# Kernel optimization log

Measured on AMD Instinct MI355X. Metric: run time of the kernel, lower is better.

The kernel has to match this reference:

```python
import jax, jax.numpy as jnp
import numpy as np

T = 8192  # context/question length (input_shape[2])
D = 128   # feature dim (input_shape[3])


def setup_inputs() -> dict:
    key = jax.random.key(0)
    k1, k2 = jax.random.split(key)
    x = jax.random.normal(k1, (2, 1, T, D), dtype=jnp.float32)
    kernel = jax.random.normal(k2, (3 * D,), dtype=jnp.float32)
    return {"x": x, "kernel": kernel}


def reference(x, kernel):
    context = x[0, 0]   # (T, D)
    question = x[1, 0]  # (T, D)
    w_c, w_q, w_m = kernel[:D], kernel[D:2 * D], kernel[2 * D:]

    # Additive similarity: S[i,j] = c_i.w_c + q_j.w_q + (c_i*q_j).w_m
    # Avoids materializing the (T, T, 3D) tiled/concatenated tensor.
    S = (context @ w_c)[:, None] + (question @ w_q)[None, :] \
        + (context * w_m) @ question.T  # (T, T)

    A = jax.nn.softmax(S, axis=-1)  # row-wise softmax, as tf.nn.softmax on 2D

    # C2Q attention: U_A[i] = sum_j A[i,j] * q_j
    U_A = A @ question  # (T, D)

    # Q2C attention: b = row-max of A, h = sum_i b_i * c_i, tiled over rows
    b = jnp.max(A, axis=1)          # (T,)
    h = b @ context                 # (D,)
    H_A = jnp.broadcast_to(h, (T, D))

    # megamerge: [c, U_A, c*U_A, c*H_A]
    G = jnp.concatenate([context, U_A, context * U_A, context * H_A], axis=-1)
    return G  # (T, 4D)
```

## Files before the change

### kernel.cpp

```cpp
#include <hip/hip_runtime.h>
#include <hip/hip_bf16.h>

#define T 8192
#define D 128
#define NSPLIT 8
#define JLEN (T / NSPLIT)
#define BN 64
#define NITER (JLEN / BN)
#define BM 128
#define LOG2E 1.44269504088896f

typedef _Float16 half4_t __attribute__((ext_vector_type(4)));
typedef _Float16 half8_t __attribute__((ext_vector_type(8)));
typedef float floatx4 __attribute__((ext_vector_type(4)));

__global__ void prep_kernel(const float* __restrict__ x, const float* __restrict__ kern,
                            _Float16* __restrict__ q16, _Float16* __restrict__ qT16,
                            _Float16* __restrict__ cm16, float* __restrict__ qq2) {
    const float* context  = x;
    const float* question = x + (size_t)T * D;
    const float* wq = kern + D;
    const float* wm = kern + 2 * D;
    __shared__ __align__(16) _Float16 tile[32][136];
    int j0 = blockIdx.x * 32;
    int t = threadIdx.x;
    int c4 = t & 31;
    int rsub = t >> 5;
    float4 wqv = ((const float4*)wq)[c4];
    float4 wmv = ((const float4*)wm)[c4];
    for (int p = 0; p < 4; ++p) {
        int row = p * 8 + rsub;
        float4 q = ((const float4*)(question + (size_t)(j0 + row) * D))[c4];
        float4 c = ((const float4*)(context  + (size_t)(j0 + row) * D))[c4];
        half4_t qh;
        qh[0] = (_Float16)q.x; qh[1] = (_Float16)q.y; qh[2] = (_Float16)q.z; qh[3] = (_Float16)q.w;
        *(half4_t*)(q16 + (size_t)(j0 + row) * D + c4 * 4) = qh;
        *(half4_t*)&tile[row][c4 * 4] = qh;
        half4_t ch;
        ch[0] = (_Float16)(c.x * wmv.x * LOG2E); ch[1] = (_Float16)(c.y * wmv.y * LOG2E);
        ch[2] = (_Float16)(c.z * wmv.z * LOG2E); ch[3] = (_Float16)(c.w * wmv.w * LOG2E);
        *(half4_t*)(cm16 + (size_t)(j0 + row) * D + c4 * 4) = ch;
        float s = q.x * wqv.x + q.y * wqv.y + q.z * wqv.z + q.w * wqv.w;
        for (int dx = 1; dx <= 16; dx <<= 1) s += __shfl_xor(s, dx);
        if (c4 == 0) qq2[j0 + row] = s * LOG2E;
    }
    __syncthreads();
    for (int p = 0; p < 2; ++p) {
        int chunk = t + p * 256;
        int d = chunk >> 2, jo = (chunk & 3) * 8;
        half8_t v;
        for (int s2 = 0; s2 < 8; ++s2) v[s2] = tile[jo + s2][d];
        *(half8_t*)(qT16 + (size_t)d * T + j0 + jo) = v;
    }
}

__global__ __launch_bounds__(256, 2)
void flash_kernel(const _Float16* __restrict__ q16, const _Float16* __restrict__ qT16,
                  const _Float16* __restrict__ cm16, const float* __restrict__ qq2,
                  unsigned char* __restrict__ Opart, float* __restrict__ mpart,
                  float* __restrict__ lpart) {
    __shared__ __align__(16) _Float16 Kt[64][144];
    __shared__ __align__(16) _Float16 Vt[128][72];
    __shared__ __align__(16) float qqs[JLEN];

    int bx = blockIdx.x;
    int rb = bx >> 3;
    int sp = bx & 7;
    int tid = threadIdx.x;
    int wave = tid >> 6;
    int lane = tid & 63;
    int quad = lane >> 4;
    int l15 = lane & 15;
    int rbase = rb * BM + wave * 32;

    ((float4*)qqs)[tid] = ((const float4*)(qq2 + (size_t)sp * JLEN))[tid];

    half8_t qfrag[2][4];
    for (int mt = 0; mt < 2; ++mt)
        for (int ks = 0; ks < 4; ++ks)
            qfrag[mt][ks] = *(const half8_t*)(cm16 + (size_t)(rbase + mt * 16 + l15) * D
                                              + ks * 32 + quad * 8);

    floatx4 acc[2][8];
    for (int mt = 0; mt < 2; ++mt)
        for (int nt = 0; nt < 8; ++nt)
            for (int r = 0; r < 4; ++r) acc[mt][nt][r] = 0.f;
    float m_run[2] = {-INFINITY, -INFINITY};
    float l_run[2] = {0.f, 0.f};

    half8_t kreg[4], vreg[4];
    {
        int j0 = sp * JLEN;
        for (int k = 0; k < 4; ++k) {
            int idx = tid + k * 256;
            kreg[k] = *(const half8_t*)(q16 + (size_t)(j0 + (idx >> 4)) * D + (idx & 15) * 8);
            vreg[k] = *(const half8_t*)(qT16 + (size_t)(idx >> 3) * T + j0 + (idx & 7) * 8);
        }
    }

    for (int it = 0; it < NITER; ++it) {
        for (int k = 0; k < 4; ++k) {
            int idx = tid + k * 256;
            *(half8_t*)&Kt[idx >> 4][(idx & 15) * 8] = kreg[k];
        }
        for (int k = 0; k < 4; ++k) {
            int idx = tid + k * 256;
            int dr = idx >> 3, c8 = idx & 7;
            int ph0 = (c8 >> 2) * 32 + (c8 & 1) * 16 + ((c8 >> 1) & 1) * 4;
            half4_t lo, hi;
            lo[0] = vreg[k][0]; lo[1] = vreg[k][1]; lo[2] = vreg[k][2]; lo[3] = vreg[k][3];
            hi[0] = vreg[k][4]; hi[1] = vreg[k][5]; hi[2] = vreg[k][6]; hi[3] = vreg[k][7];
            *(half4_t*)&Vt[dr][ph0]     = lo;
            *(half4_t*)&Vt[dr][ph0 + 8] = hi;
        }
        __syncthreads();

        if (it + 1 < NITER) {
            int j0n = sp * JLEN + (it + 1) * BN;
            for (int k = 0; k < 4; ++k) {
                int idx = tid + k * 256;
                kreg[k] = *(const half8_t*)(q16 + (size_t)(j0n + (idx >> 4)) * D + (idx & 15) * 8);
                vreg[k] = *(const half8_t*)(qT16 + (size_t)(idx >> 3) * T + j0n + (idx & 7) * 8);
            }
        }

        floatx4 St[2][4];
        for (int jt = 0; jt < 4; ++jt) {
            float4 bias = *(const float4*)&qqs[it * 64 + jt * 16 + quad * 4];
            St[0][jt][0] = bias.x; St[0][jt][1] = bias.y; St[0][jt][2] = bias.z; St[0][jt][3] = bias.w;
            St[1][jt][0] = bias.x; St[1][jt][1] = bias.y; St[1][jt][2] = bias.z; St[1][jt][3] = bias.w;
        }
        for (int ks = 0; ks < 4; ++ks)
            for (int jt = 0; jt < 4; ++jt) {
                half8_t a = *(const half8_t*)&Kt[jt * 16 + l15][ks * 32 + quad * 8];
                St[0][jt] = __builtin_amdgcn_mfma_f32_16x16x32_f16(a, qfrag[0][ks], St[0][jt], 0, 0, 0);
                St[1][jt] = __builtin_amdgcn_mfma_f32_16x16x32_f16(a, qfrag[1][ks], St[1][jt], 0, 0, 0);
            }

        half4_t apv[2][4];
        float alpha[2];
        for (int mt = 0; mt < 2; ++mt) {
            float mx = St[mt][0][0];
            for (int jt = 0; jt < 4; ++jt)
                for (int r = 0; r < 4; ++r) mx = fmaxf(mx, St[mt][jt][r]);
            mx = fmaxf(mx, __shfl_xor(mx, 16));
            mx = fmaxf(mx, __shfl_xor(mx, 32));
            float mnew = fmaxf(m_run[mt], mx);
            alpha[mt] = __builtin_amdgcn_exp2f(m_run[mt] - mnew);
            m_run[mt] = mnew;
            float ps = 0.f;
            for (int jt = 0; jt < 4; ++jt) {
                float p0 = __builtin_amdgcn_exp2f(St[mt][jt][0] - mnew);
                float p1 = __builtin_amdgcn_exp2f(St[mt][jt][1] - mnew);
                float p2 = __builtin_amdgcn_exp2f(St[mt][jt][2] - mnew);
                float p3 = __builtin_amdgcn_exp2f(St[mt][jt][3] - mnew);
                ps += (p0 + p1) + (p2 + p3);
                apv[mt][jt][0] = (_Float16)p0;
                apv[mt][jt][1] = (_Float16)p1;
                apv[mt][jt][2] = (_Float16)p2;
                apv[mt][jt][3] = (_Float16)p3;
            }
            ps += __shfl_xor(ps, 16);
            ps += __shfl_xor(ps, 32);
            l_run[mt] = l_run[mt] * alpha[mt] + ps;
        }
        for (int mt = 0; mt < 2; ++mt) {
            float aT[4];
            for (int r = 0; r < 4; ++r)
                aT[r] = __shfl(alpha[mt], quad * 4 + r);
            for (int nt = 0; nt < 8; ++nt)
                for (int r = 0; r < 4; ++r) acc[mt][nt][r] *= aT[r];
        }

        for (int pr = 0; pr < 2; ++pr) {
            for (int nt = 0; nt < 8; ++nt) {
                half8_t bb = *(const half8_t*)&Vt[nt * 16 + l15][pr * 32 + quad * 8];
                half4_t b0, b1;
                b0[0] = bb[0]; b0[1] = bb[1]; b0[2] = bb[2]; b0[3] = bb[3];
                b1[0] = bb[4]; b1[1] = bb[5]; b1[2] = bb[6]; b1[3] = bb[7];
                int jt0 = pr * 2, jt1 = pr * 2 + 1;
                acc[0][nt] = __builtin_amdgcn_mfma_f32_16x16x16f16(apv[0][jt0], b0, acc[0][nt], 0, 0, 0);
                acc[1][nt] = __builtin_amdgcn_mfma_f32_16x16x16f16(apv[1][jt0], b0, acc[1][nt], 0, 0, 0);
                acc[0][nt] = __builtin_amdgcn_mfma_f32_16x16x16f16(apv[0][jt1], b1, acc[0][nt], 0, 0, 0);
                acc[1][nt] = __builtin_amdgcn_mfma_f32_16x16x16f16(apv[1][jt1], b1, acc[1][nt], 0, 0, 0);
            }
        }
        __syncthreads();
    }

    for (int mt = 0; mt < 2; ++mt) {
        if (quad == 0) {
            int iq = rbase + mt * 16 + l15;
            mpart[(size_t)sp * T + iq] = m_run[mt];
            lpart[(size_t)sp * T + iq] = l_run[mt];
        }
        float rinv[4];
        for (int r = 0; r < 4; ++r)
            rinv[r] = 1.0f / __shfl(l_run[mt], quad * 4 + r);
        int i = rbase + mt * 16 + quad * 4;
        for (int nt = 0; nt < 8; ++nt)
            for (int r = 0; r < 4; ++r) {
                float v = acc[mt][nt][r] * rinv[r];
                int p = __builtin_amdgcn_cvt_pk_fp8_f32(v, v, 0, false);
                Opart[((size_t)sp * T + (i + r)) * D + nt * 16 + l15] = (unsigned char)(p & 0xFF);
            }
    }
}

__global__ void merge_kernel(const unsigned char* __restrict__ Opart, const float* __restrict__ mpart,
                             const float* __restrict__ lpart, float* __restrict__ U_A,
                             float* __restrict__ linv) {
    int t = threadIdx.x;
    int i = blockIdx.x * 16 + (t >> 4);
    int c = t & 15;
    float mp[NSPLIT];
    float mstar = -INFINITY;
    for (int sp = 0; sp < NSPLIT; ++sp) {
        mp[sp] = mpart[(size_t)sp * T + i];
        mstar = fmaxf(mstar, mp[sp]);
    }
    float L = 0.f;
    float u[8];
    for (int k = 0; k < 8; ++k) u[k] = 0.f;
    int d0 = c * 8;
    for (int sp = 0; sp < NSPLIT; ++sp) {
        float w = __builtin_amdgcn_exp2f(mp[sp] - mstar) * lpart[(size_t)sp * T + i];
        L += w;
        uint2 ow = *(const uint2*)(Opart + ((size_t)sp * T + i) * D + d0);
        u[0] += __builtin_amdgcn_cvt_f32_fp8(ow.x, 0) * w;
        u[1] += __builtin_amdgcn_cvt_f32_fp8(ow.x, 1) * w;
        u[2] += __builtin_amdgcn_cvt_f32_fp8(ow.x, 2) * w;
        u[3] += __builtin_amdgcn_cvt_f32_fp8(ow.x, 3) * w;
        u[4] += __builtin_amdgcn_cvt_f32_fp8(ow.y, 0) * w;
        u[5] += __builtin_amdgcn_cvt_f32_fp8(ow.y, 1) * w;
        u[6] += __builtin_amdgcn_cvt_f32_fp8(ow.y, 2) * w;
        u[7] += __builtin_amdgcn_cvt_f32_fp8(ow.y, 3) * w;
    }
    float invL = 1.0f / L;
    float4 s0 = make_float4(u[0] * invL, u[1] * invL, u[2] * invL, u[3] * invL);
    float4 s1 = make_float4(u[4] * invL, u[5] * invL, u[6] * invL, u[7] * invL);
    *(float4*)(U_A + (size_t)i * D + d0) = s0;
    *(float4*)(U_A + (size_t)i * D + d0 + 4) = s1;
    if (c == 0) linv[i] = invL;
}

__global__ void hsum_part_kernel(const float* __restrict__ x, const float* __restrict__ linv,
                                 float* __restrict__ hpart) {
    const float* context = x;
    int t = threadIdx.x;
    int d = t & 127, g = t >> 7;
    int i0 = blockIdx.x * 128 + g * 64;
    float s = 0.f;
    for (int k = 0; k < 64; ++k)
        s += context[(size_t)(i0 + k) * D + d] * linv[i0 + k];
    hpart[(size_t)(blockIdx.x * 2 + g) * 128 + d] = s;
}

__global__ void hreduce_kernel(const float* __restrict__ hpart, float* __restrict__ h) {
    int d = threadIdx.x;
    float s = 0.f;
    for (int k = 0; k < 128; ++k) s += hpart[(size_t)k * 128 + d];
    h[d] = s;
}

__global__ void assemble_kernel(const float* __restrict__ x, const float* __restrict__ U_A,
                                const float* __restrict__ h, float* __restrict__ out) {
    const float* context = x;
    int gid = blockIdx.x * 256 + threadIdx.x;
    int base = gid * 4;
    int i = base >> 9;
    int c = base & 511;
    int seg = c >> 7, d = c & 127;
    float4 r;
    if (seg == 0) {
        r = *(const float4*)(context + (size_t)i * D + d);
    } else if (seg == 1) {
        r = *(const float4*)(U_A + (size_t)i * D + d);
    } else if (seg == 2) {
        float4 a = *(const float4*)(context + (size_t)i * D + d);
        float4 b = *(const float4*)(U_A + (size_t)i * D + d);
        r = make_float4(a.x * b.x, a.y * b.y, a.z * b.z, a.w * b.w);
    } else {
        float4 a = *(const float4*)(context + (size_t)i * D + d);
        float4 b = *(const float4*)(h + d);
        r = make_float4(a.x * b.x, a.y * b.y, a.z * b.z, a.w * b.w);
    }
    *(float4*)(out + base) = r;
}

extern "C" void kernel_launch(void* const* d_in, const int* in_sizes, int n_in,
                              void* d_out, int out_size, void* d_ws, size_t ws_size,
                              hipStream_t stream) {
    const float* x = (const float*)d_in[0];
    const float* kern = (const float*)d_in[1];
    float* out = (float*)d_out;

    char* w = (char*)d_ws;
    size_t off = 0;
    _Float16* q16  = (_Float16*)(w + off); off += (size_t)T * D * 2;
    _Float16* qT16 = (_Float16*)(w + off); off += (size_t)T * D * 2;
    _Float16* cm16 = (_Float16*)(w + off); off += (size_t)T * D * 2;
    float* qq2   = (float*)(w + off); off += (size_t)T * 4;
    float* mpart = (float*)(w + off); off += (size_t)NSPLIT * T * 4;
    float* lpart = (float*)(w + off); off += (size_t)NSPLIT * T * 4;
    float* U_A   = (float*)(w + off); off += (size_t)T * D * 4;
    float* linv  = (float*)(w + off); off += (size_t)T * 4;
    float* hpart = (float*)(w + off); off += (size_t)128 * 128 * 4;
    float* h     = (float*)(w + off); off += (size_t)D * 4;

    unsigned char* Opart = (unsigned char*)d_out;

    prep_kernel<<<256, 256, 0, stream>>>(x, kern, q16, qT16, cm16, qq2);
    flash_kernel<<<512, 256, 0, stream>>>(q16, qT16, cm16, qq2, Opart, mpart, lpart);
    merge_kernel<<<512, 256, 0, stream>>>(Opart, mpart, lpart, U_A, linv);
    hsum_part_kernel<<<64, 256, 0, stream>>>(x, linv, hpart);
    hreduce_kernel<<<1, 128, 0, stream>>>(hpart, h);
    assemble_kernel<<<4096, 256, 0, stream>>>(x, U_A, h, out);
}
```

Measured before the change: 134.1 us.

## Double KV tile width and drop register prefetch in flash attention loop

Raises the key/value tile from 64 to 128 columns, so each iteration does twice the work and half as many barriers and softmax rescales. The register-staged prefetch of the next tile is removed and tiles are loaded straight from global into LDS each iteration. S is now computed per row tile (mt) to limit register pressure, and the V swizzle layout is adjusted for the wider tile. This trades lost load/compute overlap and larger LDS use (which may reduce occupancy) for fewer synchronizations.

```diff
diff --git a/kernel.cpp b/kernel.cpp
--- a/kernel.cpp
+++ b/kernel.cpp
@@ -5,7 +5,7 @@
 #define D 128
 #define NSPLIT 8
 #define JLEN (T / NSPLIT)
-#define BN 64
+#define BN 128
 #define NITER (JLEN / BN)
 #define BM 128
 #define LOG2E 1.44269504088896f
@@ -59,8 +59,8 @@
                   const _Float16* __restrict__ cm16, const float* __restrict__ qq2,
                   unsigned char* __restrict__ Opart, float* __restrict__ mpart,
                   float* __restrict__ lpart) {
-    __shared__ __align__(16) _Float16 Kt[64][144];
-    __shared__ __align__(16) _Float16 Vt[128][72];
+    __shared__ __align__(16) _Float16 Kt[128][136];
+    __shared__ __align__(16) _Float16 Vt[128][136];
     __shared__ __align__(16) float qqs[JLEN];
 
     int bx = blockIdx.x;
@@ -88,82 +88,66 @@
     float m_run[2] = {-INFINITY, -INFINITY};
     float l_run[2] = {0.f, 0.f};
 
-    half8_t kreg[4], vreg[4];
-    {
-        int j0 = sp * JLEN;
-        for (int k = 0; k < 4; ++k) {
+    for (int it = 0; it < NITER; ++it) {
+        int j0 = sp * JLEN + it * BN;
+        for (int k = 0; k < 8; ++k) {
             int idx = tid + k * 256;
-            kreg[k] = *(const half8_t*)(q16 + (size_t)(j0 + (idx >> 4)) * D + (idx & 15) * 8);
-            vreg[k] = *(const half8_t*)(qT16 + (size_t)(idx >> 3) * T + j0 + (idx & 7) * 8);
-        }
-    }
-
-    for (int it = 0; it < NITER; ++it) {
-        for (int k = 0; k < 4; ++k) {
+            int row = idx >> 4, c8 = idx & 15;
+            *(half8_t*)&Kt[row][c8 * 8] =
+                *(const half8_t*)(q16 + (size_t)(j0 + row) * D + c8 * 8);
+        }
+        for (int k = 0; k < 8; ++k) {
             int idx = tid + k * 256;
-            *(half8_t*)&Kt[idx >> 4][(idx & 15) * 8] = kreg[k];
-        }
-        for (int k = 0; k < 4; ++k) {
-            int idx = tid + k * 256;
-            int dr = idx >> 3, c8 = idx & 7;
-            int ph0 = (c8 >> 2) * 32 + (c8 & 1) * 16 + ((c8 >> 1) & 1) * 4;
+            int dr = idx >> 4, c8 = idx & 15;
+            half8_t v = *(const half8_t*)(qT16 + (size_t)dr * T + j0 + c8 * 8);
+            int pr = c8 >> 2;
+            int q0 = (2 * c8) & 3;
+            int h  = (c8 >> 1) & 1;
+            int ph0 = pr * 32 + q0 * 8 + h * 4;
             half4_t lo, hi;
-            lo[0] = vreg[k][0]; lo[1] = vreg[k][1]; lo[2] = vreg[k][2]; lo[3] = vreg[k][3];
-            hi[0] = vreg[k][4]; hi[1] = vreg[k][5]; hi[2] = vreg[k][6]; hi[3] = vreg[k][7];
+            lo[0] = v[0]; lo[1] = v[1]; lo[2] = v[2]; lo[3] = v[3];
+            hi[0] = v[4]; hi[1] = v[5]; hi[2] = v[6]; hi[3] = v[7];
             *(half4_t*)&Vt[dr][ph0]     = lo;
             *(half4_t*)&Vt[dr][ph0 + 8] = hi;
         }
         __syncthreads();
 
-        if (it + 1 < NITER) {
-            int j0n = sp * JLEN + (it + 1) * BN;
-            for (int k = 0; k < 4; ++k) {
-                int idx = tid + k * 256;
-                kreg[k] = *(const half8_t*)(q16 + (size_t)(j0n + (idx >> 4)) * D + (idx & 15) * 8);
-                vreg[k] = *(const half8_t*)(qT16 + (size_t)(idx >> 3) * T + j0n + (idx & 7) * 8);
-            }
-        }
-
-        floatx4 St[2][4];
-        for (int jt = 0; jt < 4; ++jt) {
-            float4 bias = *(const float4*)&qqs[it * 64 + jt * 16 + quad * 4];
-            St[0][jt][0] = bias.x; St[0][jt][1] = bias.y; St[0][jt][2] = bias.z; St[0][jt][3] = bias.w;
-            St[1][jt][0] = bias.x; St[1][jt][1] = bias.y; St[1][jt][2] = bias.z; St[1][jt][3] = bias.w;
-        }
-        for (int ks = 0; ks < 4; ++ks)
-            for (int jt = 0; jt < 4; ++jt) {
-                half8_t a = *(const half8_t*)&Kt[jt * 16 + l15][ks * 32 + quad * 8];
-                St[0][jt] = __builtin_amdgcn_mfma_f32_16x16x32_f16(a, qfrag[0][ks], St[0][jt], 0, 0, 0);
-                St[1][jt] = __builtin_amdgcn_mfma_f32_16x16x32_f16(a, qfrag[1][ks], St[1][jt], 0, 0, 0);
-            }
-
-        half4_t apv[2][4];
+        half4_t apv[2][8];
         float alpha[2];
         for (int mt = 0; mt < 2; ++mt) {
-            float mx = St[mt][0][0];
-            for (int jt = 0; jt < 4; ++jt)
-                for (int r = 0; r < 4; ++r) mx = fmaxf(mx, St[mt][jt][r]);
+            floatx4 St[8];
+            for (int jt = 0; jt < 8; ++jt) {
+                float4 bias = *(const float4*)&qqs[it * 128 + jt * 16 + quad * 4];
+                St[jt][0] = bias.x; St[jt][1] = bias.y; St[jt][2] = bias.z; St[jt][3] = bias.w;
+            }
+            for (int ks = 0; ks < 4; ++ks)
+                for (int jt = 0; jt < 8; ++jt) {
+                    half8_t a = *(const half8_t*)&Kt[jt * 16 + l15][ks * 32 + quad * 8];
+                    St[jt] = __builtin_amdgcn_mfma_f32_16x16x32_f16(a, qfrag[mt][ks], St[jt], 0, 0, 0);
+                }
+            float mx = St[0][0];
+            for (int jt = 0; jt < 8; ++jt)
+                for (int r = 0; r < 4; ++r) mx = fmaxf(mx, St[jt][r]);
             mx = fmaxf(mx, __shfl_xor(mx, 16));
             mx = fmaxf(mx, __shfl_xor(mx, 32));
             float mnew = fmaxf(m_run[mt], mx);
             alpha[mt] = __builtin_amdgcn_exp2f(m_run[mt] - mnew);
             m_run[mt] = mnew;
             float ps = 0.f;
-            for (int jt = 0; jt < 4; ++jt) {
-                float p0 = __builtin_amdgcn_exp2f(St[mt][jt][0] - mnew);
-                float p1 = __builtin_amdgcn_exp2f(St[mt][jt][1] - mnew);
-                float p2 = __builtin_amdgcn_exp2f(St[mt][jt][2] - mnew);
-                float p3 = __builtin_amdgcn_exp2f(St[mt][jt][3] - mnew);
+            for (int jt = 0; jt < 8; ++jt) {
+                float p0 = __builtin_amdgcn_exp2f(St[jt][0] - mnew);
+                float p1 = __builtin_amdgcn_exp2f(St[jt][1] - mnew);
+                float p2 = __builtin_amdgcn_exp2f(St[jt][2] - mnew);
+                float p3 = __builtin_amdgcn_exp2f(St[jt][3] - mnew);
                 ps += (p0 + p1) + (p2 + p3);
-                apv[mt][jt][0] = (_Float16)p0;
-                apv[mt][jt][1] = (_Float16)p1;
-                apv[mt][jt][2] = (_Float16)p2;
-                apv[mt][jt][3] = (_Float16)p3;
+                apv[mt][jt][0] = (_Float16)p0; apv[mt][jt][1] = (_Float16)p1;
+                apv[mt][jt][2] = (_Float16)p2; apv[mt][jt][3] = (_Float16)p3;
             }
             ps += __shfl_xor(ps, 16);
             ps += __shfl_xor(ps, 32);
             l_run[mt] = l_run[mt] * alpha[mt] + ps;
         }
+
         for (int mt = 0; mt < 2; ++mt) {
             float aT[4];
             for (int r = 0; r < 4; ++r)
@@ -172,7 +156,7 @@
                 for (int r = 0; r < 4; ++r) acc[mt][nt][r] *= aT[r];
         }
 
-        for (int pr = 0; pr < 2; ++pr) {
+        for (int pr = 0; pr < 4; ++pr) {
             for (int nt = 0; nt < 8; ++nt) {
                 half8_t bb = *(const half8_t*)&Vt[nt * 16 + l15][pr * 32 + quad * 8];
                 half4_t b0, b1;
```

New measurement: 137.7 us. +2.7%, slower.

## Raise flash split to 12 and trade register prefetch for occupancy

Applied to the files above, without the earlier changes.

Splits the key dimension into 12 uneven chunks of 10 or 11 tiles, launching 768 blocks instead of 512, and raises launch bounds to 3 blocks per CU. To fit the tighter register budget, it drops the register-staged prefetch of the next K/V tile and reloads the query fragments from global memory on every iteration rather than holding them in registers. The aim is more concurrent waves to hide latency and fuller use of the CUs. In exchange, loads are no longer overlapped with compute and the query fragments are re-read each tile. The larger partial-output buffer written into the output region must also still fit.

```diff
diff --git a/kernel.cpp b/kernel.cpp
--- a/kernel.cpp
+++ b/kernel.cpp
@@ -3,10 +3,8 @@
 
 #define T 8192
 #define D 128
-#define NSPLIT 8
-#define JLEN (T / NSPLIT)
+#define NSPLIT 12
 #define BN 64
-#define NITER (JLEN / BN)
 #define BM 128
 #define LOG2E 1.44269504088896f
 
@@ -54,18 +52,18 @@
     }
 }
 
-__global__ __launch_bounds__(256, 2)
+__global__ __launch_bounds__(256, 3)
 void flash_kernel(const _Float16* __restrict__ q16, const _Float16* __restrict__ qT16,
                   const _Float16* __restrict__ cm16, const float* __restrict__ qq2,
                   unsigned char* __restrict__ Opart, float* __restrict__ mpart,
                   float* __restrict__ lpart) {
     __shared__ __align__(16) _Float16 Kt[64][144];
     __shared__ __align__(16) _Float16 Vt[128][72];
-    __shared__ __align__(16) float qqs[JLEN];
+    __shared__ __align__(16) float qqs[704];
 
     int bx = blockIdx.x;
-    int rb = bx >> 3;
-    int sp = bx & 7;
+    int rb = bx / NSPLIT;
+    int sp = bx % NSPLIT;
     int tid = threadIdx.x;
     int wave = tid >> 6;
     int lane = tid & 63;
@@ -73,13 +71,14 @@
     int l15 = lane & 15;
     int rbase = rb * BM + wave * 32;
 
-    ((float4*)qqs)[tid] = ((const float4*)(qq2 + (size_t)sp * JLEN))[tid];
-
-    half8_t qfrag[2][4];
-    for (int mt = 0; mt < 2; ++mt)
-        for (int ks = 0; ks < 4; ++ks)
-            qfrag[mt][ks] = *(const half8_t*)(cm16 + (size_t)(rbase + mt * 16 + l15) * D
-                                              + ks * 32 + quad * 8);
+    int tcount = 10 + (sp < 8 ? 1 : 0);
+    int tstart = sp * 10 + (sp < 8 ? sp : 8);
+    int jbase = tstart * BN;
+
+    if (tid < tcount * 16)
+        ((float4*)qqs)[tid] = ((const float4*)(qq2 + jbase))[tid];
+
+    size_t qoff = (size_t)(rbase + l15) * D + quad * 8;
 
     floatx4 acc[2][8];
     for (int mt = 0; mt < 2; ++mt)
@@ -88,41 +87,34 @@
     float m_run[2] = {-INFINITY, -INFINITY};
     float l_run[2] = {0.f, 0.f};
 
-    half8_t kreg[4], vreg[4];
-    {
-        int j0 = sp * JLEN;
+    for (int it = 0; it < tcount; ++it) {
+        int j0 = jbase + it * BN;
+
+        const _Float16* qb = cm16;
+        asm volatile("" : "+v"(qb));
+        half8_t qf0[4], qf1[4];
+        for (int ks = 0; ks < 4; ++ks) {
+            qf0[ks] = *(const half8_t*)(qb + qoff + ks * 32);
+            qf1[ks] = *(const half8_t*)(qb + qoff + 16 * D + ks * 32);
+        }
+
         for (int k = 0; k < 4; ++k) {
             int idx = tid + k * 256;
-            kreg[k] = *(const half8_t*)(q16 + (size_t)(j0 + (idx >> 4)) * D + (idx & 15) * 8);
-            vreg[k] = *(const half8_t*)(qT16 + (size_t)(idx >> 3) * T + j0 + (idx & 7) * 8);
-        }
-    }
-
-    for (int it = 0; it < NITER; ++it) {
-        for (int k = 0; k < 4; ++k) {
-            int idx = tid + k * 256;
-            *(half8_t*)&Kt[idx >> 4][(idx & 15) * 8] = kreg[k];
+            *(half8_t*)&Kt[idx >> 4][(idx & 15) * 8] =
+                *(const half8_t*)(q16 + (size_t)(j0 + (idx >> 4)) * D + (idx & 15) * 8);
         }
         for (int k = 0; k < 4; ++k) {
             int idx = tid + k * 256;
             int dr = idx >> 3, c8 = idx & 7;
+            half8_t v = *(const half8_t*)(qT16 + (size_t)dr * T + j0 + c8 * 8);
             int ph0 = (c8 >> 2) * 32 + (c8 & 1) * 16 + ((c8 >> 1) & 1) * 4;
             half4_t lo, hi;
-            lo[0] = vreg[k][0]; lo[1] = vreg[k][1]; lo[2] = vreg[k][2]; lo[3] = vreg[k][3];
-            hi[0] = vreg[k][4]; hi[1] = vreg[k][5]; hi[2] = vreg[k][6]; hi[3] = vreg[k][7];
+            lo[0] = v[0]; lo[1] = v[1]; lo[2] = v[2]; lo[3] = v[3];
+            hi[0] = v[4]; hi[1] = v[5]; hi[2] = v[6]; hi[3] = v[7];
             *(half4_t*)&Vt[dr][ph0]     = lo;
             *(half4_t*)&Vt[dr][ph0 + 8] = hi;
         }
         __syncthreads();
-
-        if (it + 1 < NITER) {
-            int j0n = sp * JLEN + (it + 1) * BN;
-            for (int k = 0; k < 4; ++k) {
-                int idx = tid + k * 256;
-                kreg[k] = *(const half8_t*)(q16 + (size_t)(j0n + (idx >> 4)) * D + (idx & 15) * 8);
-                vreg[k] = *(const half8_t*)(qT16 + (size_t)(idx >> 3) * T + j0n + (idx & 7) * 8);
-            }
-        }
 
         floatx4 St[2][4];
         for (int jt = 0; jt < 4; ++jt) {
@@ -133,8 +125,8 @@
         for (int ks = 0; ks < 4; ++ks)
             for (int jt = 0; jt < 4; ++jt) {
                 half8_t a = *(const half8_t*)&Kt[jt * 16 + l15][ks * 32 + quad * 8];
-                St[0][jt] = __builtin_amdgcn_mfma_f32_16x16x32_f16(a, qfrag[0][ks], St[0][jt], 0, 0, 0);
-                St[1][jt] = __builtin_amdgcn_mfma_f32_16x16x32_f16(a, qfrag[1][ks], St[1][jt], 0, 0, 0);
+                St[0][jt] = __builtin_amdgcn_mfma_f32_16x16x32_f16(a, qf0[ks], St[0][jt], 0, 0, 0);
+                St[1][jt] = __builtin_amdgcn_mfma_f32_16x16x32_f16(a, qf1[ks], St[1][jt], 0, 0, 0);
             }
 
         half4_t apv[2][4];
@@ -311,7 +303,7 @@
     unsigned char* Opart = (unsigned char*)d_out;
 
     prep_kernel<<<256, 256, 0, stream>>>(x, kern, q16, qT16, cm16, qq2);
-    flash_kernel<<<512, 256, 0, stream>>>(q16, qT16, cm16, qq2, Opart, mpart, lpart);
+    flash_kernel<<<768, 256, 0, stream>>>(q16, qT16, cm16, qq2, Opart, mpart, lpart);
     merge_kernel<<<512, 256, 0, stream>>>(Opart, mpart, lpart, U_A, linv);
     hsum_part_kernel<<<64, 256, 0, stream>>>(x, linv, hpart);
     hreduce_kernel<<<1, 128, 0, stream>>>(hpart, h);
```

New measurement: 164.0 us. +22.3%, slower.

## Software-pipeline PV MFMA one iteration behind QK and softmax

Applied to the files above, without the earlier changes.

Double-buffers the V tile in shared memory and defers each iteration's P·V matrix multiply to the next iteration, so it runs after the current QK^T MFMAs and alongside the current softmax exp work. A tail block after the loop drains the last PV product. The aim is to overlap the softmax ALU/transcendental work with MFMA issue. It costs extra LDS for the second V buffer and keeps the previous P fragments live in registers, which could lower occupancy under the 2-block launch bound.

```diff
diff --git a/kernel.cpp b/kernel.cpp
--- a/kernel.cpp
+++ b/kernel.cpp
@@ -60,7 +60,7 @@
                   unsigned char* __restrict__ Opart, float* __restrict__ mpart,
                   float* __restrict__ lpart) {
     __shared__ __align__(16) _Float16 Kt[64][144];
-    __shared__ __align__(16) _Float16 Vt[128][72];
+    __shared__ __align__(16) _Float16 Vt[2][128][72];
     __shared__ __align__(16) float qqs[JLEN];
 
     int bx = blockIdx.x;
@@ -88,6 +88,9 @@
     float m_run[2] = {-INFINITY, -INFINITY};
     float l_run[2] = {0.f, 0.f};
 
+    half4_t apvP[2][4];
+    float alphaP[2];
+
     half8_t kreg[4], vreg[4];
     {
         int j0 = sp * JLEN;
@@ -99,6 +102,7 @@
     }
 
     for (int it = 0; it < NITER; ++it) {
+        int vb = it & 1;
         for (int k = 0; k < 4; ++k) {
             int idx = tid + k * 256;
             *(half8_t*)&Kt[idx >> 4][(idx & 15) * 8] = kreg[k];
@@ -110,8 +114,8 @@
             half4_t lo, hi;
             lo[0] = vreg[k][0]; lo[1] = vreg[k][1]; lo[2] = vreg[k][2]; lo[3] = vreg[k][3];
             hi[0] = vreg[k][4]; hi[1] = vreg[k][5]; hi[2] = vreg[k][6]; hi[3] = vreg[k][7];
-            *(half4_t*)&Vt[dr][ph0]     = lo;
-            *(half4_t*)&Vt[dr][ph0 + 8] = hi;
+            *(half4_t*)&Vt[vb][dr][ph0]     = lo;
+            *(half4_t*)&Vt[vb][dr][ph0 + 8] = hi;
         }
         __syncthreads();
 
@@ -137,8 +141,30 @@
                 St[1][jt] = __builtin_amdgcn_mfma_f32_16x16x32_f16(a, qfrag[1][ks], St[1][jt], 0, 0, 0);
             }
 
-        half4_t apv[2][4];
-        float alpha[2];
+        if (it > 0) {
+            int pb = vb ^ 1;
+            for (int mt = 0; mt < 2; ++mt) {
+                float aT[4];
+                for (int r = 0; r < 4; ++r)
+                    aT[r] = __shfl(alphaP[mt], quad * 4 + r);
+                for (int nt = 0; nt < 8; ++nt)
+                    for (int r = 0; r < 4; ++r) acc[mt][nt][r] *= aT[r];
+            }
+            for (int pr = 0; pr < 2; ++pr) {
+                for (int nt = 0; nt < 8; ++nt) {
+                    half8_t bb = *(const half8_t*)&Vt[pb][nt * 16 + l15][pr * 32 + quad * 8];
+                    half4_t b0, b1;
+                    b0[0] = bb[0]; b0[1] = bb[1]; b0[2] = bb[2]; b0[3] = bb[3];
+                    b1[0] = bb[4]; b1[1] = bb[5]; b1[2] = bb[6]; b1[3] = bb[7];
+                    int jt0 = pr * 2, jt1 = pr * 2 + 1;
+                    acc[0][nt] = __builtin_amdgcn_mfma_f32_16x16x16f16(apvP[0][jt0], b0, acc[0][nt], 0, 0, 0);
+                    acc[1][nt] = __builtin_amdgcn_mfma_f32_16x16x16f16(apvP[1][jt0], b0, acc[1][nt], 0, 0, 0);
+                    acc[0][nt] = __builtin_amdgcn_mfma_f32_16x16x16f16(apvP[0][jt1], b1, acc[0][nt], 0, 0, 0);
+                    acc[1][nt] = __builtin_amdgcn_mfma_f32_16x16x16f16(apvP[1][jt1], b1, acc[1][nt], 0, 0, 0);
+                }
+            }
+        }
+
         for (int mt = 0; mt < 2; ++mt) {
             float mx = St[mt][0][0];
             for (int jt = 0; jt < 4; ++jt)
@@ -146,7 +172,7 @@
             mx = fmaxf(mx, __shfl_xor(mx, 16));
             mx = fmaxf(mx, __shfl_xor(mx, 32));
             float mnew = fmaxf(m_run[mt], mx);
-            alpha[mt] = __builtin_amdgcn_exp2f(m_run[mt] - mnew);
+            alphaP[mt] = __builtin_amdgcn_exp2f(m_run[mt] - mnew);
             m_run[mt] = mnew;
             float ps = 0.f;
             for (int jt = 0; jt < 4; ++jt) {
@@ -155,37 +181,40 @@
                 float p2 = __builtin_amdgcn_exp2f(St[mt][jt][2] - mnew);
                 float p3 = __builtin_amdgcn_exp2f(St[mt][jt][3] - mnew);
                 ps += (p0 + p1) + (p2 + p3);
-                apv[mt][jt][0] = (_Float16)p0;
-                apv[mt][jt][1] = (_Float16)p1;
-                apv[mt][jt][2] = (_Float16)p2;
-                apv[mt][jt][3] = (_Float16)p3;
+                apvP[mt][jt][0] = (_Float16)p0;
+                apvP[mt][jt][1] = (_Float16)p1;
+                apvP[mt][jt][2] = (_Float16)p2;
+                apvP[mt][jt][3] = (_Float16)p3;
             }
             ps += __shfl_xor(ps, 16);
             ps += __shfl_xor(ps, 32);
-            l_run[mt] = l_run[mt] * alpha[mt] + ps;
-        }
+            l_run[mt] = l_run[mt] * alphaP[mt] + ps;
+        }
+        __syncthreads();
+    }
+
+    {
+        int pb = (NITER - 1) & 1;
         for (int mt = 0; mt < 2; ++mt) {
             float aT[4];
             for (int r = 0; r < 4; ++r)
-                aT[r] = __shfl(alpha[mt], quad * 4 + r);
+                aT[r] = __shfl(alphaP[mt], quad * 4 + r);
             for (int nt = 0; nt < 8; ++nt)
                 for (int r = 0; r < 4; ++r) acc[mt][nt][r] *= aT[r];
         }
-
         for (int pr = 0; pr < 2; ++pr) {
             for (int nt = 0; nt < 8; ++nt) {
-                half8_t bb = *(const half8_t*)&Vt[nt * 16 + l15][pr * 32 + quad * 8];
+                half8_t bb = *(const half8_t*)&Vt[pb][nt * 16 + l15][pr * 32 + quad * 8];
                 half4_t b0, b1;
                 b0[0] = bb[0]; b0[1] = bb[1]; b0[2] = bb[2]; b0[3] = bb[3];
                 b1[0] = bb[4]; b1[1] = bb[5]; b1[2] = bb[6]; b1[3] = bb[7];
                 int jt0 = pr * 2, jt1 = pr * 2 + 1;
-                acc[0][nt] = __builtin_amdgcn_mfma_f32_16x16x16f16(apv[0][jt0], b0, acc[0][nt], 0, 0, 0);
-                acc[1][nt] = __builtin_amdgcn_mfma_f32_16x16x16f16(apv[1][jt0], b0, acc[1][nt], 0, 0, 0);
-                acc[0][nt] = __builtin_amdgcn_mfma_f32_16x16x16f16(apv[0][jt1], b1, acc[0][nt], 0, 0, 0);
-                acc[1][nt] = __builtin_amdgcn_mfma_f32_16x16x16f16(apv[1][jt1], b1, acc[1][nt], 0, 0, 0);
-            }
-        }
-        __syncthreads();
+                acc[0][nt] = __builtin_amdgcn_mfma_f32_16x16x16f16(apvP[0][jt0], b0, acc[0][nt], 0, 0, 0);
+                acc[1][nt] = __builtin_amdgcn_mfma_f32_16x16x16f16(apvP[1][jt0], b0, acc[1][nt], 0, 0, 0);
+                acc[0][nt] = __builtin_amdgcn_mfma_f32_16x16x16f16(apvP[0][jt1], b1, acc[0][nt], 0, 0, 0);
+                acc[1][nt] = __builtin_amdgcn_mfma_f32_16x16x16f16(apvP[1][jt1], b1, acc[1][nt], 0, 0, 0);
+            }
+        }
     }
 
     for (int mt = 0; mt < 2; ++mt) {
```

Result: no change. 136.3 us (+1.6%).
